# Performance work log

Hardware: AMD Instinct MI355X
Metric: run time of the kernel (lower is better)

Reference implementation:

```python
import jax, jax.numpy as jnp
import numpy as np

MODEL = 2048
LATENT = 512
POS = 1024
NH = 16
HD = MODEL // NH        # 128
PHD = POS // NH         # 64
THETA = 50000.0


def _rope_tables(S, dim, base=THETA):
    inv_freq = 1.0 / (base ** (jnp.arange(0, dim, 2, dtype=jnp.float32) / dim))
    t = jnp.arange(S, dtype=jnp.float32)
    freqs = jnp.outer(t, inv_freq)                  # [S, dim/2]
    emb = jnp.concatenate([freqs, freqs], axis=-1)  # [S, dim]
    return jnp.cos(emb), jnp.sin(emb)


def _rotate_half(x):
    h = x.shape[-1] // 2
    return jnp.concatenate([-x[..., h:], x[..., :h]], axis=-1)


def _apply_rope(x, cos, sin):
    # x: [..., S, dim]; cos/sin: [S, dim]
    return x * cos + _rotate_half(x) * sin


def setup_inputs() -> dict:
    key = jax.random.key(0)
    ks = jax.random.split(key, 16)
    std = 0.02
    d = {
        'x':      jax.random.normal(ks[0], (2, 2048, MODEL), jnp.float32),
        'w_qkv':  jax.random.normal(ks[1], (MODEL, 3 * LATENT), jnp.float32) * std,
        'b_qkv':  jnp.zeros((3 * LATENT,), jnp.float32),
        'w_qup':  jax.random.normal(ks[2], (LATENT, MODEL), jnp.float32) * std,
        'b_qup':  jnp.zeros((MODEL,), jnp.float32),
        'w_kup':  jax.random.normal(ks[3], (LATENT, MODEL), jnp.float32) * std,
        'b_kup':  jnp.zeros((MODEL,), jnp.float32),
        'w_vup':  jax.random.normal(ks[4], (LATENT, MODEL), jnp.float32) * std,
        'b_vup':  jnp.zeros((MODEL,), jnp.float32),
        'w_qpos': jax.random.normal(ks[5], (LATENT, POS), jnp.float32) * std,
        'b_qpos': jnp.zeros((POS,), jnp.float32),
        'w_kpos': jax.random.normal(ks[6], (MODEL, PHD), jnp.float32) * std,
        'b_kpos': jnp.zeros((PHD,), jnp.float32),
        'w_o':    jax.random.normal(ks[7], (MODEL, MODEL), jnp.float32) * std,
        'b_o':    jnp.zeros((MODEL,), jnp.float32),
    }
    return d


def reference(x, w_qkv, b_qkv, w_qup, b_qup, w_kup, b_kup, w_vup, b_vup,
              w_qpos, b_qpos, w_kpos, b_kpos, w_o, b_o):
    B, S, _ = x.shape
    # fused down-projection into shared latent
    latent_qkv = x @ w_qkv + b_qkv                       # [B,S,3L]
    lq, lk, lv = jnp.split(latent_qkv, 3, axis=-1)       # each [B,S,L]

    cos, sin = _rope_tables(S, PHD)

    # decoupled positional key (shared across heads), RoPE on sub-slice
    pos_k = x @ w_kpos + b_kpos                          # [B,S,PHD]
    pos_k = _apply_rope(pos_k, cos, sin)

    # up-projections
    q = (lq @ w_qup + b_qup).reshape(B, S, NH, HD).transpose(0, 2, 1, 3)
    k = (lk @ w_kup + b_kup).reshape(B, S, NH, HD).transpose(0, 2, 1, 3)
    v = (lv @ w_vup + b_vup).reshape(B, S, NH, HD).transpose(0, 2, 1, 3)

    pos_q = (lq @ w_qpos + b_qpos).reshape(B, S, NH, PHD).transpose(0, 2, 1, 3)
    pos_q = _apply_rope(pos_q, cos, sin)                 # [B,NH,S,PHD]

    pos_kh = jnp.broadcast_to(pos_k[:, None], (B, NH, S, PHD))
    q = jnp.concatenate([q, pos_q], axis=-1)             # [B,NH,S,HD+PHD]
    k = jnp.concatenate([k, pos_kh], axis=-1)

    scale = 1.0 / jnp.sqrt(jnp.asarray(HD + PHD, x.dtype))
    scores = jnp.einsum('bhqd,bhkd->bhqk', q, k) * scale
    causal = jnp.tril(jnp.ones((S, S), bool))
    scores = jnp.where(causal, scores, jnp.finfo(scores.dtype).min)
    p = jax.nn.softmax(scores, axis=-1)
    attn = jnp.einsum('bhqk,bhkd->bhqd', p, v)           # [B,NH,S,HD]
    attn = attn.transpose(0, 2, 1, 3).reshape(B, S, MODEL)
    return attn @ w_o + b_o
```

## Files before the change

kernel.cpp:

```cpp
#include <hip/hip_runtime.h>
#include <cstdint>
#include <cstddef>

typedef __bf16 bf16x8 __attribute__((ext_vector_type(8)));
typedef float  f32x4  __attribute__((ext_vector_type(4)));
typedef unsigned short us8 __attribute__((ext_vector_type(8)));
typedef unsigned short us4 __attribute__((ext_vector_type(4)));

__device__ __forceinline__ unsigned short f2bf(float f) {
  union { float f; unsigned u; } v; v.f = f;
  unsigned r = v.u + 0x7FFFu + ((v.u >> 16) & 1u);
  return (unsigned short)(r >> 16);
}
__device__ __forceinline__ float b2f(unsigned short h) {
  union { unsigned u; float f; } v; v.u = ((unsigned)h) << 16;
  return v.f;
}
__device__ __forceinline__ f32x4 mfma16(bf16x8 a, bf16x8 b, f32x4 c) {
  return __builtin_amdgcn_mfma_f32_16x16x32_bf16(a, b, c, 0, 0, 0);
}
__device__ __forceinline__ void gl_lds16(const unsigned short* g, unsigned short* l) {
  __builtin_amdgcn_global_load_lds(
      (const __attribute__((address_space(1))) void*)g,
      (__attribute__((address_space(3))) void*)l, 16, 0, 0);
}

__global__ void prep_all_kernel(const float* __restrict__ b_qkv,
                                const float* __restrict__ b_kpos,
                                const float* __restrict__ b_qup,
                                const float* __restrict__ b_qpos,
                                float* __restrict__ bias1,
                                float* __restrict__ bias2q,
                                float* __restrict__ costab,
                                float* __restrict__ sintab,
                                unsigned short* __restrict__ wB1,
                                const float* __restrict__ w_qkv,
                                const float* __restrict__ w_kpos,
                                const float* __restrict__ w_qup,
                                const float* __restrict__ w_qpos,
                                const float* __restrict__ w_kup,
                                const float* __restrict__ w_vup,
                                const float* __restrict__ w_o,
                                unsigned short* __restrict__ wB2q,
                                unsigned short* __restrict__ wB2k,
                                unsigned short* __restrict__ wB2v,
                                unsigned short* __restrict__ wBo) {
  __shared__ float tile[32][33];
  int blk = blockIdx.x;
  if (blk < 512) {
    int i = blk * 256 + threadIdx.x;
    if (i < 65536) {
      int s = i >> 5, f = i & 31;
      float inv = powf(50000.0f, -(float)f / 32.0f);
      float a = (float)s * inv;
      costab[i] = cosf(a);
      sintab[i] = sinf(a);
    }
    if (i < 1664) bias1[i] = (i < 1536) ? b_qkv[i] : (i < 1600 ? b_kpos[i - 1536] : 0.0f);
    if (i < 3072) bias2q[i] = (i < 2048) ? b_qup[i] : b_qpos[i - 2048];
    if (i < 131072) wB1[(size_t)1600 * 2048 + i] = 0;
    return;
  }
  const float* in;
  unsigned short* out;
  int ldin, ldo, nx, j;
  if (blk < 3584)      { j = blk - 512;  in = w_qkv;  ldin = 1536; out = wB1;                        ldo = 2048; nx = 48; }
  else if (blk < 3712) { j = blk - 3584; in = w_kpos; ldin = 64;   out = wB1 + (size_t)1536 * 2048;  ldo = 2048; nx = 2;  }
  else if (blk < 4736) { j = blk - 3712; in = w_qup;  ldin = 2048; out = wB2q;                       ldo = 512;  nx = 64; }
  else if (blk < 5248) { j = blk - 4736; in = w_qpos; ldin = 1024; out = wB2q + (size_t)2048 * 512;  ldo = 512;  nx = 32; }
  else if (blk < 6272) { j = blk - 5248; in = w_kup;  ldin = 2048; out = wB2k;                       ldo = 512;  nx = 64; }
  else if (blk < 7296) { j = blk - 6272; in = w_vup;  ldin = 2048; out = wB2v;                       ldo = 512;  nx = 64; }
  else                 { j = blk - 7296; in = w_o;    ldin = 2048; out = wBo;                        ldo = 2048; nx = 64; }
  int c0 = (j % nx) * 32, r0 = (j / nx) * 32;
  int tx = threadIdx.x & 31, ty = threadIdx.x >> 5;
  for (int jj = 0; jj < 4; ++jj)
    tile[ty + jj * 8][tx] = in[(size_t)(r0 + ty + jj * 8) * ldin + c0 + tx];
  __syncthreads();
  for (int jj = 0; jj < 4; ++jj)
    out[(size_t)(c0 + ty + jj * 8) * ldo + r0 + tx] = f2bf(tile[tx][ty + jj * 8]);
}

__device__ __forceinline__ void xcd_decode(int nx, int& bx, int& by) {
  int bid = blockIdx.x, nwg = gridDim.x;
  int cpx = nwg >> 3;
  int wg = (bid & 7) * cpx + (bid >> 3);
  bx = wg % nx;
  by = wg / nx;
}

template <int OUT_MODE>
__global__ __launch_bounds__(256, 2)
void gemm_bt_kernel(const unsigned short* __restrict__ A, int lda,
                    const unsigned short* __restrict__ Bt, int ldb,
                    void* __restrict__ Cout, int ldc,
                    const float* __restrict__ bias, int K, int nx) {
  __shared__ unsigned short smem[32768];
  int tid = threadIdx.x;
  int wave = tid >> 6, lane = tid & 63;
  int g = lane >> 4, r = lane & 15;
  int wr = wave >> 1, wc = wave & 1;
  int bx, by;
  xcd_decode(nx, bx, by);
  long brow = (long)by * 128, bcol = (long)bx * 128;

  int srowl = lane >> 3;
  int sw = ((lane & 7) ^ (srowl & 7)) * 8;
  const unsigned short* Abase = A + (brow + wave * 32 + srowl) * (long)lda + sw;
  const unsigned short* Bbase = Bt + (bcol + wave * 32 + srowl) * (long)ldb + sw;

  f32x4 acc[4][4];
  for (int mi = 0; mi < 4; ++mi)
    for (int ni = 0; ni < 4; ++ni)
      acc[mi][ni] = f32x4{0.f, 0.f, 0.f, 0.f};

  auto stage = [&](int buf, int k0) {
    unsigned short* ab = smem + buf * 16384;
    unsigned short* bb = ab + 8192;
    for (int c = 0; c < 4; ++c) {
      gl_lds16(Abase + (size_t)c * 8 * lda + k0, ab + (wave * 32 + c * 8) * 64);
      gl_lds16(Bbase + (size_t)c * 8 * ldb + k0, bb + (wave * 32 + c * 8) * 64);
    }
  };

  int rx = (r & 7) << 4;
  int nt = K >> 6;

  stage(0, 0);
  for (int t = 0; t < nt; ++t) {
    if (t + 1 < nt) {
      stage((t + 1) & 1, (t + 1) << 6);
      asm volatile("s_waitcnt vmcnt(8)" ::: "memory");
    } else {
      asm volatile("s_waitcnt vmcnt(0)" ::: "memory");
    }
    __builtin_amdgcn_sched_barrier(0);
    __builtin_amdgcn_s_barrier();
    __builtin_amdgcn_sched_barrier(0);
    const char* Ab = (const char*)(smem + (t & 1) * 16384);
    const char* Bb = Ab + 16384;
    for (int kk = 0; kk < 2; ++kk) {
      bf16x8 af[4], bfv[4];
      for (int mi = 0; mi < 4; ++mi)
        af[mi] = *(const bf16x8*)(Ab + (size_t)(wr * 64 + mi * 16 + r) * 128 +
                                  ((kk * 64 + g * 16) ^ rx));
      for (int ni = 0; ni < 4; ++ni)
        bfv[ni] = *(const bf16x8*)(Bb + (size_t)(wc * 64 + ni * 16 + r) * 128 +
                                   ((kk * 64 + g * 16) ^ rx));
      for (int mi = 0; mi < 4; ++mi)
        for (int ni = 0; ni < 4; ++ni)
          acc[mi][ni] = mfma16(af[mi], bfv[ni], acc[mi][ni]);
    }
    __builtin_amdgcn_sched_barrier(0);
    __builtin_amdgcn_s_barrier();
  }

  if (OUT_MODE == 2) {
    for (int mi = 0; mi < 4; ++mi)
      for (int ni = 0; ni < 4; ++ni) {
        int col = wc * 64 + ni * 16 + r;
        float bv = bias[bcol + col];
        int rowb = wr * 64 + mi * 16 + g * 4;
        for (int i = 0; i < 4; ++i)
          smem[col * 136 + rowb + i] = f2bf(acc[mi][ni][i] + bv);
      }
    __syncthreads();
    int col = tid >> 1, half = tid & 1;
    int bh = (int)(brow >> 11) * 16 + (int)(bcol >> 7);
    unsigned short* outp = (unsigned short*)Cout +
                           ((size_t)bh * 128 + col) * 2048 + (brow & 2047);
    for (int j = 0; j < 8; ++j) {
      int row0 = half * 64 + j * 8;
      *(us8*)(outp + row0) = *(const us8*)&smem[col * 136 + row0];
    }
    return;
  }

  for (int mi = 0; mi < 4; ++mi)
    for (int ni = 0; ni < 4; ++ni) {
      long col = bcol + wc * 64 + ni * 16 + r;
      float bv = bias ? bias[col] : 0.0f;
      long rowb = brow + wr * 64 + mi * 16 + g * 4;
      for (int i = 0; i < 4; ++i) {
        float v = acc[mi][ni][i] + bv;
        if (OUT_MODE == 1)
          ((float*)Cout)[(rowb + i) * (long)ldc + col] = v;
        else
          ((unsigned short*)Cout)[(rowb + i) * (long)ldc + col] = f2bf(v);
      }
    }
}

__global__ __launch_bounds__(256, 2)
void gemm_a32_kernel(const float* __restrict__ A, int lda,
                     const unsigned short* __restrict__ Bt, int ldb,
                     unsigned short* __restrict__ Cout, int ldc,
                     const float* __restrict__ bias, int K, int nx) {
  __shared__ unsigned short smem[32768];
  int tid = threadIdx.x;
  int wave = tid >> 6, lane = tid & 63;
  int g = lane >> 4, r = lane & 15;
  int wr = wave >> 1, wc = wave & 1;
  int bx, by;
  xcd_decode(nx, bx, by);
  long brow = (long)by * 128, bcol = (long)bx * 128;

  int f4c = tid & 15, row0 = tid >> 4;
  int ablk = f4c >> 1, asub = (f4c & 1) * 8;
  const float4* Ag = (const float4*)(A + (brow + row0) * (size_t)lda) + f4c;

  int srowl = lane >> 3;
  int sw = ((lane & 7) ^ (srowl & 7)) * 8;
  const unsigned short* Bbase = Bt + (bcol + wave * 32 + srowl) * (long)ldb + sw;

  f32x4 acc[4][4];
  for (int mi = 0; mi < 4; ++mi)
    for (int ni = 0; ni < 4; ++ni)
      acc[mi][ni] = f32x4{0.f, 0.f, 0.f, 0.f};

  auto stage_b = [&](int buf, int k0) {
    unsigned short* bb = smem + 16384 + buf * 8192;
    for (int c = 0; c < 4; ++c)
      gl_lds16(Bbase + (size_t)c * 8 * ldb + k0, bb + (wave * 32 + c * 8) * 64);
  };

  int rx = (r & 7) << 4;
  int nt = K >> 6;

  float4 areg[8];
#pragma unroll
  for (int s = 0; s < 8; ++s) areg[s] = Ag[(size_t)s * 8192];
  stage_b(0, 0);

  for (int t = 0; t < nt; ++t) {
    char* alds = (char*)(smem + (t & 1) * 8192);
#pragma unroll
    for (int s = 0; s < 8; ++s) {
      us4 hv;
      hv[0] = f2bf(areg[s].x); hv[1] = f2bf(areg[s].y);
      hv[2] = f2bf(areg[s].z); hv[3] = f2bf(areg[s].w);
      int row = row0 + s * 16;
      *(us4*)(alds + row * 128 + ((ablk ^ (row & 7)) << 4) + asub) = hv;
    }
    asm volatile("s_waitcnt vmcnt(0)" ::: "memory");
    asm volatile("s_waitcnt lgkmcnt(0)" ::: "memory");
    __builtin_amdgcn_sched_barrier(0);
    __builtin_amdgcn_s_barrier();
    __builtin_amdgcn_sched_barrier(0);
    if (t + 1 < nt) {
      int k1 = (t + 1) << 6;
#pragma unroll
      for (int s = 0; s < 8; ++s) areg[s] = Ag[(size_t)s * 8192 + (k1 >> 2)];
      stage_b((t + 1) & 1, k1);
    }
    const char* Ab = (const char*)(smem + (t & 1) * 8192);
    const char* Bb = (const char*)(smem + 16384 + (t & 1) * 8192);
    for (int kk = 0; kk < 2; ++kk) {
      bf16x8 af[4], bfv[4];
      for (int mi = 0; mi < 4; ++mi)
        af[mi] = *(const bf16x8*)(Ab + (size_t)(wr * 64 + mi * 16 + r) * 128 +
                                  ((kk * 64 + g * 16) ^ rx));
      for (int ni = 0; ni < 4; ++ni)
        bfv[ni] = *(const bf16x8*)(Bb + (size_t)(wc * 64 + ni * 16 + r) * 128 +
                                   ((kk * 64 + g * 16) ^ rx));
      for (int mi = 0; mi < 4; ++mi)
        for (int ni = 0; ni < 4; ++ni)
          acc[mi][ni] = mfma16(af[mi], bfv[ni], acc[mi][ni]);
    }
    __builtin_amdgcn_sched_barrier(0);
    __builtin_amdgcn_s_barrier();
  }

  for (int mi = 0; mi < 4; ++mi)
    for (int ni = 0; ni < 4; ++ni) {
      long col = bcol + wc * 64 + ni * 16 + r;
      float bv = bias[col];
      long rowb = brow + wr * 64 + mi * 16 + g * 4;
      for (int i = 0; i < 4; ++i)
        Cout[(rowb + i) * (long)ldc + col] = f2bf(acc[mi][ni][i] + bv);
    }
}

__global__ void rope_kernel(const unsigned short* __restrict__ tmp_q,
                            const unsigned short* __restrict__ latext,
                            const float* __restrict__ costab,
                            const float* __restrict__ sintab,
                            unsigned short* __restrict__ posqr,
                            unsigned short* __restrict__ poskr) {
  int idx = blockIdx.x * 256 + threadIdx.x;
  const unsigned short* src;
  unsigned short* dst;
  int s, dp0;
  if (idx < 524288) {
    int rowA = idx >> 7, rem = idx & 127;
    int h = rem >> 3;
    dp0 = (rem & 7) * 8;
    s = rowA & 2047;
    src = tmp_q + (size_t)rowA * 3072 + 2048 + h * 64;
    dst = posqr + (size_t)rowA * 1024 + h * 64 + dp0;
  } else if (idx < 557056) {
    int j = idx - 524288;
    int rowA = j >> 3;
    dp0 = (j & 7) * 8;
    s = rowA & 2047;
    src = latext + (size_t)rowA * 1664 + 1536;
    dst = poskr + (size_t)rowA * 64 + dp0;
  } else {
    return;
  }
  us8 x1 = *(const us8*)(src + dp0);
  us8 x2 = *(const us8*)(src + (dp0 ^ 32));
  int f0 = dp0 & 31;
  const float* cp = costab + s * 32 + f0;
  const float* sp = sintab + s * 32 + f0;
  bool low = dp0 < 32;
  us8 o;
  for (int e = 0; e < 8; ++e) {
    float a = b2f(x1[e]), b = b2f(x2[e]);
    float v = low ? (a * cp[e] - b * sp[e]) : (a * cp[e] + b * sp[e]);
    o[e] = f2bf(v);
  }
  *(us8*)dst = o;
}

__device__ __forceinline__ void task_decode(int t, int& qt, int& seg, int& bh) {
  if (t < 1024) {
    qt = 31 - (t >> 7); int rem = t & 127; seg = rem >> 5; bh = rem & 31;
  } else if (t < 1792) {
    int t2 = t - 1024; int qi = t2 / 96; int rem = t2 - qi * 96;
    qt = 23 - qi; seg = rem >> 5; bh = rem & 31;
  } else if (t < 2304) {
    int t3 = t - 1792; qt = 15 - (t3 >> 6); int rem = t3 & 63; seg = rem >> 5; bh = rem & 31;
  } else {
    int t4 = t - 2304; qt = 7 - (t4 >> 5); seg = 0; bh = t4 & 31;
  }
}
__device__ __forceinline__ int task_slot(int qt, int seg, int bh) {
  if (qt >= 24) return (31 - qt) * 128 + seg * 32 + bh;
  if (qt >= 16) return 1024 + (23 - qt) * 96 + seg * 32 + bh;
  return 1792 + (15 - qt) * 64 + seg * 32 + bh;
}

__global__ __launch_bounds__(256, 2)
void flash_kernel(const unsigned short* __restrict__ tmp_q,
                  const unsigned short* __restrict__ tmp_k,
                  const unsigned short* __restrict__ posqr,
                  const unsigned short* __restrict__ poskr,
                  const unsigned short* __restrict__ vT,
                  unsigned short* __restrict__ ob,
                  unsigned short* __restrict__ Opart,
                  float* __restrict__ mlbuf,
                  int* __restrict__ counter) {
  const int S = 2048;
  int tid = threadIdx.x, wave = tid >> 6, lane = tid & 63;
  int g = lane >> 4, r = lane & 15;
  const float sl2 = 1.44269504f / 13.8564064605510183f;
  const float DEFER = 96.0f;

  __shared__ unsigned short Klds[32 * 192];
  __shared__ unsigned short Vlds[128 * 32];
  __shared__ unsigned short Plds[4][16][40];
  __shared__ int s_tile;
  char* Kb = (char*)Klds;
  char* Vb = (char*)Vlds;
  int rx7 = (r & 7) << 4, rx3 = (r & 3) << 4;

  us8 onesu;
  for (int e = 0; e < 8; ++e) onesu[e] = 0x3F80;
  bf16x8 ones = *(const bf16x8*)&onesu;

  int kn_row[2], kn_seg[2];
  for (int j = 0; j < 2; ++j) {
    int slot = j * 256 + tid;
    kn_row[j] = slot >> 4;
    kn_seg[j] = slot & 15;
  }
  int kr_row = tid >> 3, kr_seg = tid & 7;
  int v_row[2], v_seg[2];
  for (int j = 0; j < 2; ++j) {
    int slot = j * 256 + tid;
    v_row[j] = slot >> 2;
    v_seg[j] = slot & 3;
  }

  for (;;) {
    if (tid == 0) s_tile = atomicAdd(counter, 1);
    __syncthreads();
    int t = s_tile;
    if (t >= 2560) return;
    int qt, seg, bh;
    task_decode(t, qt, seg, bh);
    int b = bh >> 4, h = bh & 15;
    int qbase = qt * 64;
    int cbeg = seg * 16;
    int cend = min(cbeg + 16, 2 * (qt + 1));
    size_t rb = (size_t)b * 2048;

    const unsigned short* kpn = tmp_k + rb * 2048 + h * 128;
    const unsigned short* kpr = poskr + rb * 64;
    const unsigned short* vp = vT + (size_t)bh * 128 * S;

    bf16x8 qf[6];
    {
      size_t qrowA = rb + qbase + wave * 16 + r;
      const unsigned short* qn = tmp_q + qrowA * 3072 + h * 128 + g * 8;
      for (int c = 0; c < 4; ++c) qf[c] = *(const bf16x8*)(qn + c * 32);
      const unsigned short* qr_ = posqr + qrowA * 1024 + h * 64 + g * 8;
      qf[4] = *(const bf16x8*)(qr_);
      qf[5] = *(const bf16x8*)(qr_ + 32);
    }

    f32x4 acc[8];
    for (int d = 0; d < 8; ++d) acc[d] = f32x4{0.f, 0.f, 0.f, 0.f};
    f32x4 lacc = {0.f, 0.f, 0.f, 0.f};
    float m_r[4];
    for (int i = 0; i < 4; ++i) m_r[i] = -3.0e38f;

    us8 kreg[2], krope, vreg[2];
    {
      int kv0 = cbeg * 32;
      for (int j = 0; j < 2; ++j)
        kreg[j] = *(const us8*)(kpn + (size_t)(kv0 + kn_row[j]) * 2048 + kn_seg[j] * 8);
      krope = *(const us8*)(kpr + (size_t)(kv0 + kr_row) * 64 + kr_seg * 8);
      for (int j = 0; j < 2; ++j)
        vreg[j] = *(const us8*)(vp + (size_t)v_row[j] * S + kv0 + v_seg[j] * 8);
    }

    for (int ch = cbeg; ch < cend; ++ch) {
      for (int j = 0; j < 2; ++j)
        *(us8*)(Kb + (size_t)kn_row[j] * 384 +
                ((kn_seg[j] ^ (kn_row[j] & 7)) << 4)) = kreg[j];
      *(us8*)(Kb + (size_t)kr_row * 384 +
              (((16 + kr_seg) ^ (kr_row & 7)) << 4)) = krope;
      for (int j = 0; j < 2; ++j)
        *(us8*)(Vb + (size_t)v_row[j] * 64 +
                ((v_seg[j] ^ (v_row[j] & 3)) << 4)) = vreg[j];
      asm volatile("s_waitcnt lgkmcnt(0)" ::: "memory");
      __builtin_amdgcn_sched_barrier(0);
      __builtin_amdgcn_s_barrier();
      __builtin_amdgcn_sched_barrier(0);
      if (ch + 1 < cend) {
        int kv1 = (ch + 1) * 32;
        for (int j = 0; j < 2; ++j)
          kreg[j] = *(const us8*)(kpn + (size_t)(kv1 + kn_row[j]) * 2048 + kn_seg[j] * 8);
        krope = *(const us8*)(kpr + (size_t)(kv1 + kr_row) * 64 + kr_seg * 8);
        for (int j = 0; j < 2; ++j)
          vreg[j] = *(const us8*)(vp + (size_t)v_row[j] * S + kv1 + v_seg[j] * 8);
      }
      int kv0 = ch * 32;

      f32x4 sc0 = {0.f, 0.f, 0.f, 0.f}, sc1 = {0.f, 0.f, 0.f, 0.f};
      __builtin_amdgcn_s_setprio(1);
      for (int c = 0; c < 6; ++c) {
        bf16x8 kf0 = *(const bf16x8*)(Kb + (size_t)r * 384 + (((c * 4 + g) << 4) ^ rx7));
        sc0 = mfma16(qf[c], kf0, sc0);
      }
      for (int c = 0; c < 6; ++c) {
        bf16x8 kf1 = *(const bf16x8*)(Kb + (size_t)(16 + r) * 384 + (((c * 4 + g) << 4) ^ rx7));
        sc1 = mfma16(qf[c], kf1, sc1);
      }
      __builtin_amdgcn_s_setprio(0);

      int qi_min = qbase + wave * 16;
      if (kv0 + 31 > qi_min) {
        int kj0 = kv0 + r, kj1 = kv0 + 16 + r;
        int qi0 = qi_min + g * 4;
        for (int i = 0; i < 4; ++i) {
          if (kj0 > qi0 + i) sc0[i] = -1e30f;
          if (kj1 > qi0 + i) sc1[i] = -1e30f;
        }
      }

      float tl[4];
      bool ok = true;
      for (int i = 0; i < 4; ++i) {
        tl[i] = fmaxf(sc0[i], sc1[i]);
        ok = ok && (tl[i] - m_r[i] <= DEFER);
      }
      if (!__all(ok)) {
        for (int i = 0; i < 4; ++i) {
          float tm = tl[i];
          for (int off = 1; off < 16; off <<= 1) tm = fmaxf(tm, __shfl_xor(tm, off, 64));
          float mnew = fmaxf(m_r[i], tm);
          float corr = exp2f((m_r[i] - mnew) * sl2);
          lacc[i] *= corr;
          for (int d = 0; d < 8; ++d) acc[d][i] *= corr;
          m_r[i] = mnew;
        }
      }
      float p0[4], p1[4];
      for (int i = 0; i < 4; ++i) {
        p0[i] = exp2f((sc0[i] - m_r[i]) * sl2);
        p1[i] = exp2f((sc1[i] - m_r[i]) * sl2);
      }

      for (int i = 0; i < 4; ++i) {
        Plds[wave][g * 4 + i][r] = f2bf(p0[i]);
        Plds[wave][g * 4 + i][16 + r] = f2bf(p1[i]);
      }
      bf16x8 pa = *(const bf16x8*)&Plds[wave][r][g * 8];
      __builtin_amdgcn_s_setprio(1);
      lacc = mfma16(pa, ones, lacc);
      for (int dt = 0; dt < 8; ++dt) {
        bf16x8 vf = *(const bf16x8*)(Vb + (size_t)(dt * 16 + r) * 64 + ((g << 4) ^ rx3));
        acc[dt] = mfma16(pa, vf, acc[dt]);
      }
      __builtin_amdgcn_s_setprio(0);
      __builtin_amdgcn_sched_barrier(0);
      __builtin_amdgcn_s_barrier();
    }

    if (qt <= 7) {
      for (int i = 0; i < 4; ++i) {
        float inv = 1.0f / lacc[i];
        int row = qbase + wave * 16 + g * 4 + i;
        size_t base = (rb + row) * 2048 + h * 128;
        for (int dt = 0; dt < 8; ++dt)
          ob[base + dt * 16 + r] = f2bf(acc[dt][i] * inv);
      }
    } else {
      unsigned short* op = Opart + (size_t)t * 8192;
      for (int i = 0; i < 4; ++i) {
        int row = wave * 16 + g * 4 + i;
        for (int dt = 0; dt < 8; ++dt)
          op[row * 128 + dt * 16 + r] = f2bf(acc[dt][i]);
        if (r == 0) {
          mlbuf[(size_t)t * 128 + row * 2]     = m_r[i];
          mlbuf[(size_t)t * 128 + row * 2 + 1] = lacc[i];
        }
      }
    }
  }
}

__global__ void merge_kernel(const unsigned short* __restrict__ Opart,
                             const float* __restrict__ mlbuf,
                             unsigned short* __restrict__ ob) {
  int qt = 8 + (blockIdx.x >> 5), bh = blockIdx.x & 31;
  int b = bh >> 4, h = bh & 15;
  int tid = threadIdx.x;
  int row = tid >> 2, c0 = (tid & 3) * 32;
  const float sl2 = 1.44269504f / 13.8564064605510183f;
  int ns = (qt >= 24) ? 4 : (qt >= 16 ? 3 : 2);

  size_t slot[4];
  float m[4], l[4], w[4];
  float M = -3.0e38f;
#pragma unroll
  for (int j = 0; j < 4; ++j) {
    if (j < ns) {
      slot[j] = task_slot(qt, j, bh);
      m[j] = mlbuf[slot[j] * 128 + row * 2];
      l[j] = mlbuf[slot[j] * 128 + row * 2 + 1];
      M = fmaxf(M, m[j]);
    }
  }
  float L = 0.f;
#pragma unroll
  for (int j = 0; j < 4; ++j)
    if (j < ns) { w[j] = exp2f((m[j] - M) * sl2); L += w[j] * l[j]; }
  float invL = 1.f / L;
#pragma unroll
  for (int j = 0; j < 4; ++j) if (j < ns) w[j] *= invL;

  float o[32];
#pragma unroll
  for (int e = 0; e < 32; ++e) o[e] = 0.f;
#pragma unroll
  for (int j = 0; j < 4; ++j) {
    if (j < ns) {
      const unsigned short* pp = Opart + slot[j] * 8192 + row * 128 + c0;
      for (int blk = 0; blk < 4; ++blk) {
        us8 v = *(const us8*)(pp + blk * 8);
        for (int e = 0; e < 8; ++e) o[blk * 8 + e] += w[j] * b2f(v[e]);
      }
    }
  }
  size_t obase = ((size_t)b * 2048 + qt * 64 + row) * 2048 + h * 128 + c0;
  for (int blk = 0; blk < 4; ++blk) {
    us8 st;
    for (int e = 0; e < 8; ++e) st[e] = f2bf(o[blk * 8 + e]);
    *(us8*)(ob + obase + blk * 8) = st;
  }
}

extern "C" void kernel_launch(void* const* d_in, const int* in_sizes, int n_in,
                              void* d_out, int out_size, void* d_ws, size_t ws_size,
                              hipStream_t stream) {
  const float* x      = (const float*)d_in[0];
  const float* w_qkv  = (const float*)d_in[1];
  const float* b_qkv  = (const float*)d_in[2];
  const float* w_qup  = (const float*)d_in[3];
  const float* b_qup  = (const float*)d_in[4];
  const float* w_kup  = (const float*)d_in[5];
  const float* b_kup  = (const float*)d_in[6];
  const float* w_vup  = (const float*)d_in[7];
  const float* b_vup  = (const float*)d_in[8];
  const float* w_qpos = (const float*)d_in[9];
  const float* b_qpos = (const float*)d_in[10];
  const float* w_kpos = (const float*)d_in[11];
  const float* b_kpos = (const float*)d_in[12];
  const float* w_o    = (const float*)d_in[13];
  const float* b_o    = (const float*)d_in[14];
  (void)in_sizes; (void)n_in; (void)out_size; (void)ws_size;

  char* ws = (char*)d_ws;
  size_t off = 0;
  auto alloc = [&](size_t bytes) -> char* {
    char* p = ws + off;
    off += (bytes + 255) & ~(size_t)255;
    return p;
  };

  unsigned short* wB1    = (unsigned short*)alloc(6815744);
  unsigned short* wB2q   = (unsigned short*)alloc(3145728);
  unsigned short* wB2k   = (unsigned short*)alloc(2097152);
  unsigned short* wB2v   = (unsigned short*)alloc(2097152);
  unsigned short* wBo    = (unsigned short*)alloc(8388608);
  float*          bias1  = (float*)alloc(1664 * 4);
  float*          bias2q = (float*)alloc(3072 * 4);
  float*          costab = (float*)alloc(262144);
  float*          sintab = (float*)alloc(262144);
  unsigned short* latext = (unsigned short*)alloc(13631488);
  unsigned short* tmp_q  = (unsigned short*)alloc(25165824);
  unsigned short* tmp_k  = (unsigned short*)alloc(16777216);
  unsigned short* vTbuf  = (unsigned short*)alloc(16777216);
  unsigned short* posqr  = (unsigned short*)alloc(8388608);
  unsigned short* poskr  = (unsigned short*)alloc(524288);
  unsigned short* Opart  = (unsigned short*)alloc(41943040);
  float*          mlbuf  = (float*)alloc(1310720);
  int*            counter= (int*)alloc(256);
  unsigned short* attnb  = (unsigned short*)alloc(16777216);

  prep_all_kernel<<<11392, 256, 0, stream>>>(b_qkv, b_kpos, b_qup, b_qpos,
                                             bias1, bias2q, costab, sintab, wB1,
                                             w_qkv, w_kpos, w_qup, w_qpos, w_kup,
                                             w_vup, w_o, wB2q, wB2k, wB2v, wBo);
  gemm_a32_kernel<<<416, 256, 0, stream>>>(x, 2048, wB1, 2048,
                                           latext, 1664, bias1, 2048, 13);
  gemm_bt_kernel<0><<<768, 256, 0, stream>>>(latext, 1664, wB2q, 512,
                                             tmp_q, 3072, bias2q, 512, 24);
  gemm_bt_kernel<0><<<512, 256, 0, stream>>>(latext + 512, 1664, wB2k, 512,
                                             tmp_k, 2048, b_kup, 512, 16);
  gemm_bt_kernel<2><<<512, 256, 0, stream>>>(latext + 1024, 1664, wB2v, 512,
                                             vTbuf, 2048, b_vup, 512, 16);
  rope_kernel<<<2176, 256, 0, stream>>>(tmp_q, latext, costab, sintab, posqr, poskr);
  hipMemsetAsync(counter, 0, 4, stream);
  flash_kernel<<<1280, 256, 0, stream>>>(tmp_q, tmp_k, posqr, poskr, vTbuf,
                                         attnb, Opart, mlbuf, counter);
  merge_kernel<<<768, 256, 0, stream>>>(Opart, mlbuf, attnb);
  gemm_bt_kernel<1><<<512, 256, 0, stream>>>(attnb, 2048, wBo, 2048,
                                             d_out, 2048, b_o, 2048, 16);
}
```

Before: 281.5 us.

## Split flash work queue into 8 per-XCD queues grouped by batch-head

Replaces the single global atomic task counter with eight queues, each covering a subset of batch-head pairs. Blocks start on the queue matching blockIdx&7 and move to the others once theirs is drained. The aim is to keep each batch-head's K/V reads local to one XCD's L2 and to spread contention on the atomic counter. It adds an extra __syncthreads per task fetch, and the mapping of blocks to XCDs is assumed rather than guaranteed, which can hurt load balance near the tail.

Result: slower. 374.5 us (+33.0%).

```diff
diff --git a/kernel.cpp b/kernel.cpp
--- a/kernel.cpp
+++ b/kernel.cpp
@@ -322,22 +322,20 @@
   *(us8*)dst = o;
 }
 
-__device__ __forceinline__ void task_decode(int t, int& qt, int& seg, int& bh) {
-  if (t < 1024) {
-    qt = 31 - (t >> 7); int rem = t & 127; seg = rem >> 5; bh = rem & 31;
-  } else if (t < 1792) {
-    int t2 = t - 1024; int qi = t2 / 96; int rem = t2 - qi * 96;
-    qt = 23 - qi; seg = rem >> 5; bh = rem & 31;
-  } else if (t < 2304) {
-    int t3 = t - 1792; qt = 15 - (t3 >> 6); int rem = t3 & 63; seg = rem >> 5; bh = rem & 31;
-  } else {
-    int t4 = t - 2304; qt = 7 - (t4 >> 5); seg = 0; bh = t4 & 31;
-  }
-}
 __device__ __forceinline__ int task_slot(int qt, int seg, int bh) {
   if (qt >= 24) return (31 - qt) * 128 + seg * 32 + bh;
   if (qt >= 16) return 1024 + (23 - qt) * 96 + seg * 32 + bh;
   return 1792 + (15 - qt) * 64 + seg * 32 + bh;
+}
+
+__device__ __forceinline__ void queue_decode(int q, int i, int& qt, int& seg, int& bh) {
+  int bsel = i / 80;
+  int p = i - bsel * 80;
+  bh = q + bsel * 8;
+  if (p < 32)      { qt = 31 - (p >> 2); seg = p & 3; }
+  else if (p < 56) { int p2 = p - 32; int d = p2 / 3; qt = 23 - d; seg = p2 - d * 3; }
+  else if (p < 72) { int p3 = p - 56; qt = 15 - (p3 >> 1); seg = p3 & 1; }
+  else             { qt = 7 - (p - 72); seg = 0; }
 }
 
 __global__ __launch_bounds__(256, 2)
@@ -349,7 +347,7 @@
                   unsigned short* __restrict__ ob,
                   unsigned short* __restrict__ Opart,
                   float* __restrict__ mlbuf,
-                  int* __restrict__ counter) {
+                  int* __restrict__ counters) {
   const int S = 2048;
   int tid = threadIdx.x, wave = tid >> 6, lane = tid & 63;
   int g = lane >> 4, r = lane & 15;
@@ -382,150 +380,156 @@
     v_seg[j] = slot & 3;
   }
 
-  for (;;) {
-    if (tid == 0) s_tile = atomicAdd(counter, 1);
-    __syncthreads();
-    int t = s_tile;
-    if (t >= 2560) return;
-    int qt, seg, bh;
-    task_decode(t, qt, seg, bh);
-    int b = bh >> 4, h = bh & 15;
-    int qbase = qt * 64;
-    int cbeg = seg * 16;
-    int cend = min(cbeg + 16, 2 * (qt + 1));
-    size_t rb = (size_t)b * 2048;
-
-    const unsigned short* kpn = tmp_k + rb * 2048 + h * 128;
-    const unsigned short* kpr = poskr + rb * 64;
-    const unsigned short* vp = vT + (size_t)bh * 128 * S;
-
-    bf16x8 qf[6];
-    {
-      size_t qrowA = rb + qbase + wave * 16 + r;
-      const unsigned short* qn = tmp_q + qrowA * 3072 + h * 128 + g * 8;
-      for (int c = 0; c < 4; ++c) qf[c] = *(const bf16x8*)(qn + c * 32);
-      const unsigned short* qr_ = posqr + qrowA * 1024 + h * 64 + g * 8;
-      qf[4] = *(const bf16x8*)(qr_);
-      qf[5] = *(const bf16x8*)(qr_ + 32);
-    }
-
-    f32x4 acc[8];
-    for (int d = 0; d < 8; ++d) acc[d] = f32x4{0.f, 0.f, 0.f, 0.f};
-    f32x4 lacc = {0.f, 0.f, 0.f, 0.f};
-    float m_r[4];
-    for (int i = 0; i < 4; ++i) m_r[i] = -3.0e38f;
-
-    us8 kreg[2], krope, vreg[2];
-    {
-      int kv0 = cbeg * 32;
-      for (int j = 0; j < 2; ++j)
-        kreg[j] = *(const us8*)(kpn + (size_t)(kv0 + kn_row[j]) * 2048 + kn_seg[j] * 8);
-      krope = *(const us8*)(kpr + (size_t)(kv0 + kr_row) * 64 + kr_seg * 8);
-      for (int j = 0; j < 2; ++j)
-        vreg[j] = *(const us8*)(vp + (size_t)v_row[j] * S + kv0 + v_seg[j] * 8);
-    }
-
-    for (int ch = cbeg; ch < cend; ++ch) {
-      for (int j = 0; j < 2; ++j)
-        *(us8*)(Kb + (size_t)kn_row[j] * 384 +
-                ((kn_seg[j] ^ (kn_row[j] & 7)) << 4)) = kreg[j];
-      *(us8*)(Kb + (size_t)kr_row * 384 +
-              (((16 + kr_seg) ^ (kr_row & 7)) << 4)) = krope;
-      for (int j = 0; j < 2; ++j)
-        *(us8*)(Vb + (size_t)v_row[j] * 64 +
-                ((v_seg[j] ^ (v_row[j] & 3)) << 4)) = vreg[j];
-      asm volatile("s_waitcnt lgkmcnt(0)" ::: "memory");
-      __builtin_amdgcn_sched_barrier(0);
-      __builtin_amdgcn_s_barrier();
-      __builtin_amdgcn_sched_barrier(0);
-      if (ch + 1 < cend) {
-        int kv1 = (ch + 1) * 32;
+  int myq = blockIdx.x & 7;
+  for (int qq = 0; qq < 8; ++qq) {
+    int q = (myq + qq) & 7;
+    for (;;) {
+      if (tid == 0) s_tile = atomicAdd(&counters[q], 1);
+      __syncthreads();
+      int ti = s_tile;
+      __syncthreads();
+      if (ti >= 320) break;
+      int qt, seg, bh;
+      queue_decode(q, ti, qt, seg, bh);
+      int b = bh >> 4, h = bh & 15;
+      int qbase = qt * 64;
+      int cbeg = seg * 16;
+      int cend = min(cbeg + 16, 2 * (qt + 1));
+      size_t rb = (size_t)b * 2048;
+
+      const unsigned short* kpn = tmp_k + rb * 2048 + h * 128;
+      const unsigned short* kpr = poskr + rb * 64;
+      const unsigned short* vp = vT + (size_t)bh * 128 * S;
+
+      bf16x8 qf[6];
+      {
+        size_t qrowA = rb + qbase + wave * 16 + r;
+        const unsigned short* qn = tmp_q + qrowA * 3072 + h * 128 + g * 8;
+        for (int c = 0; c < 4; ++c) qf[c] = *(const bf16x8*)(qn + c * 32);
+        const unsigned short* qr_ = posqr + qrowA * 1024 + h * 64 + g * 8;
+        qf[4] = *(const bf16x8*)(qr_);
+        qf[5] = *(const bf16x8*)(qr_ + 32);
+      }
+
+      f32x4 acc[8];
+      for (int d = 0; d < 8; ++d) acc[d] = f32x4{0.f, 0.f, 0.f, 0.f};
+      f32x4 lacc = {0.f, 0.f, 0.f, 0.f};
+      float m_r[4];
+      for (int i = 0; i < 4; ++i) m_r[i] = -3.0e38f;
+
+      us8 kreg[2], krope, vreg[2];
+      {
+        int kv0 = cbeg * 32;
         for (int j = 0; j < 2; ++j)
-          kreg[j] = *(const us8*)(kpn + (size_t)(kv1 + kn_row[j]) * 2048 + kn_seg[j] * 8);
-        krope = *(const us8*)(kpr + (size_t)(kv1 + kr_row) * 64 + kr_seg * 8);
+          kreg[j] = *(const us8*)(kpn + (size_t)(kv0 + kn_row[j]) * 2048 + kn_seg[j] * 8);
+        krope = *(const us8*)(kpr + (size_t)(kv0 + kr_row) * 64 + kr_seg * 8);
         for (int j = 0; j < 2; ++j)
-          vreg[j] = *(const us8*)(vp + (size_t)v_row[j] * S + kv1 + v_seg[j] * 8);
+          vreg[j] = *(const us8*)(vp + (size_t)v_row[j] * S + kv0 + v_seg[j] * 8);
       }
-      int kv0 = ch * 32;
-
-      f32x4 sc0 = {0.f, 0.f, 0.f, 0.f}, sc1 = {0.f, 0.f, 0.f, 0.f};
-      __builtin_amdgcn_s_setprio(1);
-      for (int c = 0; c < 6; ++c) {
-        bf16x8 kf0 = *(const bf16x8*)(Kb + (size_t)r * 384 + (((c * 4 + g) << 4) ^ rx7));
-        sc0 = mfma16(qf[c], kf0, sc0);
+
+      for (int ch = cbeg; ch < cend; ++ch) {
+        for (int j = 0; j < 2; ++j)
+          *(us8*)(Kb + (size_t)kn_row[j] * 384 +
+                  ((kn_seg[j] ^ (kn_row[j] & 7)) << 4)) = kreg[j];
+        *(us8*)(Kb + (size_t)kr_row * 384 +
+                (((16 + kr_seg) ^ (kr_row & 7)) << 4)) = krope;
+        for (int j = 0; j < 2; ++j)
+          *(us8*)(Vb + (size_t)v_row[j] * 64 +
+                  ((v_seg[j] ^ (v_row[j] & 3)) << 4)) = vreg[j];
+        asm volatile("s_waitcnt lgkmcnt(0)" ::: "memory");
+        __builtin_amdgcn_sched_barrier(0);
+        __builtin_amdgcn_s_barrier();
+        __builtin_amdgcn_sched_barrier(0);
+        if (ch + 1 < cend) {
+          int kv1 = (ch + 1) * 32;
+          for (int j = 0; j < 2; ++j)
+            kreg[j] = *(const us8*)(kpn + (size_t)(kv1 + kn_row[j]) * 2048 + kn_seg[j] * 8);
+          krope = *(const us8*)(kpr + (size_t)(kv1 + kr_row) * 64 + kr_seg * 8);
+          for (int j = 0; j < 2; ++j)
+            vreg[j] = *(const us8*)(vp + (size_t)v_row[j] * S + kv1 + v_seg[j] * 8);
+        }
+        int kv0 = ch * 32;
+
+        f32x4 sc0 = {0.f, 0.f, 0.f, 0.f}, sc1 = {0.f, 0.f, 0.f, 0.f};
+        __builtin_amdgcn_s_setprio(1);
+        for (int c = 0; c < 6; ++c) {
+          bf16x8 kf0 = *(const bf16x8*)(Kb + (size_t)r * 384 + (((c * 4 + g) << 4) ^ rx7));
+          sc0 = mfma16(qf[c], kf0, sc0);
+        }
+        for (int c = 0; c < 6; ++c) {
+          bf16x8 kf1 = *(const bf16x8*)(Kb + (size_t)(16 + r) * 384 + (((c * 4 + g) << 4) ^ rx7));
+          sc1 = mfma16(qf[c], kf1, sc1);
+        }
+        __builtin_amdgcn_s_setprio(0);
+
+        int qi_min = qbase + wave * 16;
+        if (kv0 + 31 > qi_min) {
+          int kj0 = kv0 + r, kj1 = kv0 + 16 + r;
+          int qi0 = qi_min + g * 4;
+          for (int i = 0; i < 4; ++i) {
+            if (kj0 > qi0 + i) sc0[i] = -1e30f;
+            if (kj1 > qi0 + i) sc1[i] = -1e30f;
+          }
+        }
+
+        float tl[4];
+        bool ok = true;
+        for (int i = 0; i < 4; ++i) {
+          tl[i] = fmaxf(sc0[i], sc1[i]);
+          ok = ok && (tl[i] - m_r[i] <= DEFER);
+        }
+        if (!__all(ok)) {
+          for (int i = 0; i < 4; ++i) {
+            float tm = tl[i];
+            for (int off = 1; off < 16; off <<= 1) tm = fmaxf(tm, __shfl_xor(tm, off, 64));
+            float mnew = fmaxf(m_r[i], tm);
+            float corr = exp2f((m_r[i] - mnew) * sl2);
+            lacc[i] *= corr;
+            for (int d = 0; d < 8; ++d) acc[d][i] *= corr;
+            m_r[i] = mnew;
+          }
+        }
+        float p0[4], p1[4];
+        for (int i = 0; i < 4; ++i) {
+          p0[i] = exp2f((sc0[i] - m_r[i]) * sl2);
+          p1[i] = exp2f((sc1[i] - m_r[i]) * sl2);
+        }
+
+        for (int i = 0; i < 4; ++i) {
+          Plds[wave][g * 4 + i][r] = f2bf(p0[i]);
+          Plds[wave][g * 4 + i][16 + r] = f2bf(p1[i]);
+        }
+        bf16x8 pa = *(const bf16x8*)&Plds[wave][r][g * 8];
+        __builtin_amdgcn_s_setprio(1);
+        lacc = mfma16(pa, ones, lacc);
+        for (int dt = 0; dt < 8; ++dt) {
+          bf16x8 vf = *(const bf16x8*)(Vb + (size_t)(dt * 16 + r) * 64 + ((g << 4) ^ rx3));
+          acc[dt] = mfma16(pa, vf, acc[dt]);
+        }
+        __builtin_amdgcn_s_setprio(0);
+        __builtin_amdgcn_sched_barrier(0);
+        __builtin_amdgcn_s_barrier();
       }
-      for (int c = 0; c < 6; ++c) {
-        bf16x8 kf1 = *(const bf16x8*)(Kb + (size_t)(16 + r) * 384 + (((c * 4 + g) << 4) ^ rx7));
-        sc1 = mfma16(qf[c], kf1, sc1);
-      }
-      __builtin_amdgcn_s_setprio(0);
-
-      int qi_min = qbase + wave * 16;
-      if (kv0 + 31 > qi_min) {
-        int kj0 = kv0 + r, kj1 = kv0 + 16 + r;
-        int qi0 = qi_min + g * 4;
+
+      if (qt <= 7) {
         for (int i = 0; i < 4; ++i) {
-          if (kj0 > qi0 + i) sc0[i] = -1e30f;
-          if (kj1 > qi0 + i) sc1[i] = -1e30f;
-        }
-      }
-
-      float tl[4];
-      bool ok = true;
-      for (int i = 0; i < 4; ++i) {
-        tl[i] = fmaxf(sc0[i], sc1[i]);
-        ok = ok && (tl[i] - m_r[i] <= DEFER);
-      }
-      if (!__all(ok)) {
+          float inv = 1.0f / lacc[i];
+          int row = qbase + wave * 16 + g * 4 + i;
+          size_t base = (rb + row) * 2048 + h * 128;
+          for (int dt = 0; dt < 8; ++dt)
+            ob[base + dt * 16 + r] = f2bf(acc[dt][i] * inv);
+        }
+      } else {
+        int slot = task_slot(qt, seg, bh);
+        unsigned short* op = Opart + (size_t)slot * 8192;
         for (int i = 0; i < 4; ++i) {
-          float tm = tl[i];
-          for (int off = 1; off < 16; off <<= 1) tm = fmaxf(tm, __shfl_xor(tm, off, 64));
-          float mnew = fmaxf(m_r[i], tm);
-          float corr = exp2f((m_r[i] - mnew) * sl2);
-          lacc[i] *= corr;
-          for (int d = 0; d < 8; ++d) acc[d][i] *= corr;
-          m_r[i] = mnew;
-        }
-      }
-      float p0[4], p1[4];
-      for (int i = 0; i < 4; ++i) {
-        p0[i] = exp2f((sc0[i] - m_r[i]) * sl2);
-        p1[i] = exp2f((sc1[i] - m_r[i]) * sl2);
-      }
-
-      for (int i = 0; i < 4; ++i) {
-        Plds[wave][g * 4 + i][r] = f2bf(p0[i]);
-        Plds[wave][g * 4 + i][16 + r] = f2bf(p1[i]);
-      }
-      bf16x8 pa = *(const bf16x8*)&Plds[wave][r][g * 8];
-      __builtin_amdgcn_s_setprio(1);
-      lacc = mfma16(pa, ones, lacc);
-      for (int dt = 0; dt < 8; ++dt) {
-        bf16x8 vf = *(const bf16x8*)(Vb + (size_t)(dt * 16 + r) * 64 + ((g << 4) ^ rx3));
-        acc[dt] = mfma16(pa, vf, acc[dt]);
-      }
-      __builtin_amdgcn_s_setprio(0);
-      __builtin_amdgcn_sched_barrier(0);
-      __builtin_amdgcn_s_barrier();
-    }
-
-    if (qt <= 7) {
-      for (int i = 0; i < 4; ++i) {
-        float inv = 1.0f / lacc[i];
-        int row = qbase + wave * 16 + g * 4 + i;
-        size_t base = (rb + row) * 2048 + h * 128;
-        for (int dt = 0; dt < 8; ++dt)
-          ob[base + dt * 16 + r] = f2bf(acc[dt][i] * inv);
-      }
-    } else {
-      unsigned short* op = Opart + (size_t)t * 8192;
-      for (int i = 0; i < 4; ++i) {
-        int row = wave * 16 + g * 4 + i;
-        for (int dt = 0; dt < 8; ++dt)
-          op[row * 128 + dt * 16 + r] = f2bf(acc[dt][i]);
-        if (r == 0) {
-          mlbuf[(size_t)t * 128 + row * 2]     = m_r[i];
-          mlbuf[(size_t)t * 128 + row * 2 + 1] = lacc[i];
+          int row = wave * 16 + g * 4 + i;
+          for (int dt = 0; dt < 8; ++dt)
+            op[row * 128 + dt * 16 + r] = f2bf(acc[dt][i]);
+          if (r == 0) {
+            mlbuf[(size_t)slot * 128 + row * 2]     = m_r[i];
+            mlbuf[(size_t)slot * 128 + row * 2 + 1] = lacc[i];
+          }
         }
       }
     }
@@ -628,7 +632,7 @@
   unsigned short* poskr  = (unsigned short*)alloc(524288);
   unsigned short* Opart  = (unsigned short*)alloc(41943040);
   float*          mlbuf  = (float*)alloc(1310720);
-  int*            counter= (int*)alloc(256);
+  int*            counters = (int*)alloc(256);
   unsigned short* attnb  = (unsigned short*)alloc(16777216);
 
   prep_all_kernel<<<11392, 256, 0, stream>>>(b_qkv, b_kpos, b_qup, b_qpos,
@@ -644,9 +648,9 @@
   gemm_bt_kernel<2><<<512, 256, 0, stream>>>(latext + 1024, 1664, wB2v, 512,
                                              vTbuf, 2048, b_vup, 512, 16);
   rope_kernel<<<2176, 256, 0, stream>>>(tmp_q, latext, costab, sintab, posqr, poskr);
-  hipMemsetAsync(counter, 0, 4, stream);
+  hipMemsetAsync(counters, 0, 256, stream);
   flash_kernel<<<1280, 256, 0, stream>>>(tmp_q, tmp_k, posqr, poskr, vTbuf,
-                                         attnb, Opart, mlbuf, counter);
+                                         attnb, Opart, mlbuf, counters);
   merge_kernel<<<768, 256, 0, stream>>>(Opart, mlbuf, attnb);
   gemm_bt_kernel<1><<<512, 256, 0, stream>>>(attnb, 2048, wBo, 2048,
                                              d_out, 2048, b_o, 2048, 16);
```
